# Performance work log

Hardware: AMD Instinct MI355X
Metric: run time of the kernel (lower is better)

Reference implementation:

```python
import jax, jax.numpy as jnp
import numpy as np
import math

L, N, D = 1024, 64, 64
O = 1024

def setup_inputs() -> dict:
    key = jax.random.key(0)
    k1, k2 = jax.random.split(key)
    x = jax.random.normal(k1, (L, N, D), dtype=jnp.float32)
    upfold = jax.random.normal(k2, (O, N, D), dtype=jnp.float32)
    return {"x": x, "upfold": upfold}

def reference(x, upfold):
    # x: [L, N, D], upfold: [O, N, D]
    d = x.shape[-1]
    scale = 1.0 / math.sqrt(d)
    # affinities: [L, O, N]
    affinities = jnp.einsum('lnd,ond->lon', x, upfold) * scale
    # weighted sum with (sigmoid - 0.5) weights: [L, N, D]
    features = jnp.einsum('lon,ond->lnd', jax.nn.sigmoid(affinities) - 0.5, upfold)
    return features
```

## Files before the change

kernel.cpp:

```cpp
#include <hip/hip_runtime.h>
#include <stdint.h>

#define L_DIM 1024
#define N_DIM 64
#define D_DIM 64
#define O_DIM 1024
#define ND    4096
#define NT    8

typedef float    floatx16 __attribute__((ext_vector_type(16)));
typedef _Float16 half8    __attribute__((ext_vector_type(8)));
typedef _Float16 h2       __attribute__((ext_vector_type(2)));
typedef __fp16   fp16x2   __attribute__((ext_vector_type(2)));

#define IMG_TILE 19
#undef IMG_TILE
#define UB_BYTES  9216
#define UTT_BYTES 9728
#define IMG_BYTES (UB_BYTES + UTT_BYTES)
#define WS_NEEDED ((size_t)N_DIM * 16 * IMG_BYTES)

#define BUF_STRIDE_FB 17920

__device__ __forceinline__ uint32_t pkh2(float a, float b) {
    fp16x2 p = __builtin_amdgcn_cvt_pkrtz(a, b);
    return __builtin_bit_cast(uint32_t, p);
}

__device__ __forceinline__ half8 mk_frag(uint32_t a, uint32_t b, uint32_t c, uint32_t d) {
    union { uint32_t u[4]; half8 v; } U;
    U.u[0] = a; U.u[1] = b; U.u[2] = c; U.u[3] = d;
    return U.v;
}

__device__ __forceinline__ uint32_t psig(float s0, float s1) {
    const h2 HI = {(_Float16)41.6f,        (_Float16)41.6f};
    const h2 LO = {(_Float16)-41.6f,       (_Float16)-41.6f};
    const h2 SC = {(_Float16)0.0625f,      (_Float16)0.0625f};
    const h2 C0 = {(_Float16)0.03099238f,  (_Float16)0.03099238f};
    const h2 C1 = {(_Float16)-0.00842090f, (_Float16)-0.00842090f};
    const h2 C2 = {(_Float16)0.00151845f,  (_Float16)0.00151845f};
    const h2 C3 = {(_Float16)-1.02197e-4f, (_Float16)-1.02197e-4f};
    h2 s = __builtin_bit_cast(h2, pkh2(s0, s1));
    s = __builtin_elementwise_min(s, HI);
    s = __builtin_elementwise_max(s, LO);
    h2 ha = s * SC;
    h2 v  = ha * ha;
    h2 w  = C2 + v * C3;
    w     = C1 + v * w;
    w     = C0 + v * w;
    h2 f  = s * w;
    return __builtin_bit_cast(uint32_t, f);
}

__device__ __forceinline__ void load_tile(const float* ubase, int ot,
                                          int r8, int c, float4* va, float4* vb) {
    const float* pr = ubase + (size_t)(ot * 64 + 2 * r8) * ND + 4 * c;
    #pragma unroll
    for (int j = 0; j < 2; ++j) {
        va[j] = *(const float4*)(pr + (size_t)(32 * j) * ND);
        vb[j] = *(const float4*)(pr + (size_t)(32 * j) * ND + ND);
    }
}

__device__ __forceinline__ void gll16(const unsigned char* g, unsigned char* l) {
    __builtin_amdgcn_global_load_lds(
        (const __attribute__((address_space(1))) void*)g,
        (__attribute__((address_space(3))) void*)l, 16, 0, 0);
}

__global__ void __launch_bounds__(256)
conv_kernel(const float* __restrict__ up, unsigned char* __restrict__ img)
{
    const int tid = threadIdx.x;
    const int r8  = tid >> 4;
    const int c   = tid & 15;
    const int n   = blockIdx.x;
    const int ot  = blockIdx.y;

    const float* ubase = up + (size_t)n * D_DIM;
    float4 va[2], vb[2];
    load_tile(ubase, ot, r8, c, va, vb);

    unsigned char* tb = img + (size_t)(n * 16 + ot) * IMG_BYTES;
    uint16_t (*Ub)[72]  = (uint16_t (*)[72])tb;
    uint32_t (*UtT)[38] = (uint32_t (*)[38])(tb + UB_BYTES);

    #pragma unroll
    for (int j = 0; j < 2; ++j) {
        *(uint2*)&Ub[2*r8 + 32*j][4*c] =
            make_uint2(pkh2(va[j].x, va[j].y), pkh2(va[j].z, va[j].w));
        *(uint2*)&Ub[2*r8 + 32*j + 1][4*c] =
            make_uint2(pkh2(vb[j].x, vb[j].y), pkh2(vb[j].z, vb[j].w));
        const int op = r8 + 16*j;
        UtT[4*c + 0][op] = pkh2(va[j].x, vb[j].x);
        UtT[4*c + 1][op] = pkh2(va[j].y, vb[j].y);
        UtT[4*c + 2][op] = pkh2(va[j].z, vb[j].z);
        UtT[4*c + 3][op] = pkh2(va[j].w, vb[j].w);
    }
}

__global__ void __launch_bounds__(512, 4)
corr_kernel_g(const float* __restrict__ x, const unsigned char* __restrict__ img,
              float* __restrict__ out)
{
    __shared__ __align__(16) unsigned char smem[4 * IMG_BYTES];

    const int tid  = threadIdx.x;
    const int lane = tid & 63;
    const int wid  = tid >> 6;
    const int team = wid >> 2;
    const int tw   = wid & 3;
    const int l31  = lane & 31;
    const int h    = lane >> 5;
    const int ttid = tid & 255;
    const int n    = blockIdx.x;
    const int lb   = blockIdx.y;
    const int lw   = lb * 128 + tw * 32 + l31;

    const int ob = team * NT;
    unsigned char* tsmem = smem + team * 2 * IMG_BYTES;
    const unsigned char* gimg = img + (size_t)n * 16 * IMG_BYTES;

    half8 Xf[4];
    {
        float (*Xs)[68] = (float (*)[68])smem;
        const int xr = tid >> 2;
        const int xq = tid & 3;
        const float* xsrc = x + (size_t)(lb * 128 + xr) * ND + n * D_DIM;
        #pragma unroll
        for (int j = 0; j < 4; ++j) {
            const int f4i = xq * 4 + j;
            *(float4*)&Xs[xr][4 * f4i] = *(const float4*)(xsrc + 4 * f4i);
        }
        __syncthreads();
        const int rl = tw * 32 + l31;
        #pragma unroll
        for (int kk = 0; kk < 4; ++kk) {
            float4 f1 = *(const float4*)&Xs[rl][16 * kk + 8 * h];
            float4 f2 = *(const float4*)&Xs[rl][16 * kk + 8 * h + 4];
            Xf[kk] = mk_frag(pkh2(f1.x, f1.y), pkh2(f1.z, f1.w),
                             pkh2(f2.x, f2.y), pkh2(f2.z, f2.w));
        }
        __syncthreads();
    }

    {
        const unsigned char* g0 = gimg + (size_t)ob * IMG_BYTES;
        #pragma unroll
        for (int i = 0; i < 4; ++i)
            gll16(g0 + ttid * 16 + i * 4096, tsmem + tw * 1024 + i * 4096);
        if (ttid < 160)
            gll16(g0 + ttid * 16 + 16384, tsmem + tw * 1024 + 16384);
    }
    __syncthreads();

    floatx16 F0, F1;
    #pragma unroll
    for (int i = 0; i < 16; ++i) { F0[i] = 0.0f; F1[i] = 0.0f; }

    for (int ot = 0; ot < NT; ++ot) {
        const int b = ot & 1;
        const unsigned char* bufc = tsmem + b * IMG_BYTES;
        unsigned char*       bufn = tsmem + (b ^ 1) * IMG_BYTES;
        const uint16_t (*Ub)[72] = (const uint16_t (*)[72])bufc;
        const uint32_t* utT      = (const uint32_t*)(bufc + UB_BYTES);

        if (ot + 1 < NT) {
            const unsigned char* gn = gimg + (size_t)(ob + ot + 1) * IMG_BYTES;
            #pragma unroll
            for (int i = 0; i < 4; ++i)
                gll16(gn + ttid * 16 + i * 4096, bufn + tw * 1024 + i * 4096);
            if (ttid < 160)
                gll16(gn + ttid * 16 + 16384, bufn + tw * 1024 + 16384);
        }

        half8 A0k[4], A1k[4];
        #pragma unroll
        for (int kk = 0; kk < 4; ++kk) {
            A0k[kk] = *(const half8*)&Ub[l31][16 * kk + 8 * h];
            A1k[kk] = *(const half8*)&Ub[32 + l31][16 * kk + 8 * h];
        }

        floatx16 S0, S1;
        #pragma unroll
        for (int i = 0; i < 16; ++i) { S0[i] = 0.0f; S1[i] = 0.0f; }
        #pragma unroll
        for (int kk = 0; kk < 4; ++kk) {
            S0 = __builtin_amdgcn_mfma_f32_32x32x16_f16(A0k[kk], Xf[kk], S0, 0, 0, 0);
            S1 = __builtin_amdgcn_mfma_f32_32x32x16_f16(A1k[kk], Xf[kk], S1, 0, 0, 0);
        }

        uint32_t P[16];
        #pragma unroll
        for (int m = 0; m < 8; ++m) P[m]     = psig(S0[2*m], S0[2*m+1]);
        #pragma unroll
        for (int m = 0; m < 8; ++m) P[8 + m] = psig(S1[2*m], S1[2*m+1]);

        uint32_t R[8];
        #pragma unroll
        for (int c2 = 0; c2 < 4; ++c2) {
            const uint32_t* Q = P + (c2 >> 1) * 8;
            const int t4 = (c2 & 1) * 4;
            R[2*c2]   = __shfl_xor(h ? Q[t4]     : Q[t4 + 2], 32);
            R[2*c2+1] = __shfl_xor(h ? Q[t4 + 1] : Q[t4 + 3], 32);
        }
        #pragma unroll
        for (int c2 = 0; c2 < 4; ++c2) {
            const uint32_t* Q = P + (c2 >> 1) * 8;
            const int t4 = (c2 & 1) * 4;
            half8 B = h ? mk_frag(R[2*c2], R[2*c2+1], Q[t4 + 2], Q[t4 + 3])
                        : mk_frag(Q[t4], Q[t4 + 1], R[2*c2], R[2*c2+1]);
            const int opb = 8 * c2 + 4 * h;
            const uint32_t* r0 = utT + l31 * 38;
            const uint32_t* r1 = utT + (32 + l31) * 38;
            uint2 q0 = *(const uint2*)(r0 + opb);
            uint2 q1 = *(const uint2*)(r0 + opb + 2);
            uint2 q2 = *(const uint2*)(r1 + opb);
            uint2 q3 = *(const uint2*)(r1 + opb + 2);
            half8 A0 = mk_frag(q0.x, q0.y, q1.x, q1.y);
            half8 A1 = mk_frag(q2.x, q2.y, q3.x, q3.y);
            F0 = __builtin_amdgcn_mfma_f32_32x32x16_f16(A0, B, F0, 0, 0, 0);
            F1 = __builtin_amdgcn_mfma_f32_32x32x16_f16(A1, B, F1, 0, 0, 0);
        }
        __syncthreads();
    }

    {
        float (*Fs)[68] = (float (*)[68])smem;
        const int row = tw * 32 + l31;
        if (team == 1) {
            #pragma unroll
            for (int q = 0; q < 4; ++q) {
                float4 a; a.x = F0[4*q]; a.y = F0[4*q+1]; a.z = F0[4*q+2]; a.w = F0[4*q+3];
                *(float4*)&Fs[row][8*q + 4*h] = a;
                float4 bq; bq.x = F1[4*q]; bq.y = F1[4*q+1]; bq.z = F1[4*q+2]; bq.w = F1[4*q+3];
                *(float4*)&Fs[row][32 + 8*q + 4*h] = bq;
            }
        }
        __syncthreads();
        if (team == 0) {
            float* op = out + (size_t)lw * ND + n * D_DIM;
            #pragma unroll
            for (int q = 0; q < 4; ++q) {
                float4 t0 = *(const float4*)&Fs[row][8*q + 4*h];
                float4 a; a.x = F0[4*q]   + t0.x; a.y = F0[4*q+1] + t0.y;
                          a.z = F0[4*q+2] + t0.z; a.w = F0[4*q+3] + t0.w;
                *(float4*)(op + 8*q + 4*h) = a;
                float4 t1 = *(const float4*)&Fs[row][32 + 8*q + 4*h];
                float4 bq; bq.x = F1[4*q]   + t1.x; bq.y = F1[4*q+1] + t1.y;
                           bq.z = F1[4*q+2] + t1.z; bq.w = F1[4*q+3] + t1.w;
                *(float4*)(op + 32 + 8*q + 4*h) = bq;
            }
        }
    }
}

__global__ void __launch_bounds__(512, 4)
corr_kernel_fb(const float* __restrict__ x, const float* __restrict__ up,
               float* __restrict__ out)
{
    __shared__ __align__(16) unsigned char smem[4 * BUF_STRIDE_FB];

    const int tid  = threadIdx.x;
    const int lane = tid & 63;
    const int wid  = tid >> 6;
    const int team = wid >> 2;
    const int tw   = wid & 3;
    const int l31  = lane & 31;
    const int h    = lane >> 5;
    const int ttid = tid & 255;
    const int r8   = ttid >> 4;
    const int c    = ttid & 15;
    const int n    = blockIdx.x;
    const int lb   = blockIdx.y;
    const int lw   = lb * 128 + tw * 32 + l31;

    const float* ubase = up + (size_t)n * D_DIM;
    const int ob = team * NT;
    unsigned char* tsmem = smem + team * 2 * BUF_STRIDE_FB;

    float4 va[2], vb[2];
    load_tile(ubase, ob + 0, r8, c, va, vb);

    half8 Xf[4];
    {
        float (*Xs)[68] = (float (*)[68])smem;
        const int xr = tid >> 2;
        const int xq = tid & 3;
        const float* xsrc = x + (size_t)(lb * 128 + xr) * ND + n * D_DIM;
        #pragma unroll
        for (int j = 0; j < 4; ++j) {
            const int f4i = xq * 4 + j;
            *(float4*)&Xs[xr][4 * f4i] = *(const float4*)(xsrc + 4 * f4i);
        }
        __syncthreads();
        const int rl = tw * 32 + l31;
        #pragma unroll
        for (int kk = 0; kk < 4; ++kk) {
            float4 f1 = *(const float4*)&Xs[rl][16 * kk + 8 * h];
            float4 f2 = *(const float4*)&Xs[rl][16 * kk + 8 * h + 4];
            Xf[kk] = mk_frag(pkh2(f1.x, f1.y), pkh2(f1.z, f1.w),
                             pkh2(f2.x, f2.y), pkh2(f2.z, f2.w));
        }
        __syncthreads();
    }

    #pragma unroll
    for (int j = 0; j < 2; ++j) {
        uint16_t (*Ub)[72]  = (uint16_t (*)[72])(tsmem);
        uint32_t (*Ut2)[68] = (uint32_t (*)[68])(tsmem + 9216);
        *(uint2*)&Ub[2*r8 + 32*j][4*c] =
            make_uint2(pkh2(va[j].x, va[j].y), pkh2(va[j].z, va[j].w));
        *(uint2*)&Ub[2*r8 + 32*j + 1][4*c] =
            make_uint2(pkh2(vb[j].x, vb[j].y), pkh2(vb[j].z, vb[j].w));
        *(uint4*)&Ut2[r8 + 16*j][4*c] =
            make_uint4(pkh2(va[j].x, vb[j].x), pkh2(va[j].y, vb[j].y),
                       pkh2(va[j].z, vb[j].z), pkh2(va[j].w, vb[j].w));
    }
    load_tile(ubase, ob + 1, r8, c, va, vb);
    __syncthreads();

    floatx16 F0, F1;
    #pragma unroll
    for (int i = 0; i < 16; ++i) { F0[i] = 0.0f; F1[i] = 0.0f; }

    for (int ot = 0; ot < NT; ++ot) {
        const int b = ot & 1;
        uint16_t (*Ub)[72]   = (uint16_t (*)[72])(tsmem + b * BUF_STRIDE_FB);
        const uint32_t* utp  = (const uint32_t*)(tsmem + b * BUF_STRIDE_FB + 9216);
        uint16_t (*Ubn)[72]  = (uint16_t (*)[72])(tsmem + (b ^ 1) * BUF_STRIDE_FB);
        uint32_t (*Ut2n)[68] = (uint32_t (*)[68])(tsmem + (b ^ 1) * BUF_STRIDE_FB + 9216);

        half8 A0k[4], A1k[4];
        #pragma unroll
        for (int kk = 0; kk < 4; ++kk) {
            A0k[kk] = *(const half8*)&Ub[l31][16 * kk + 8 * h];
            A1k[kk] = *(const half8*)&Ub[32 + l31][16 * kk + 8 * h];
        }

        if (ot + 1 < NT) {
            #pragma unroll
            for (int j = 0; j < 2; ++j) {
                *(uint2*)&Ubn[2*r8 + 32*j][4*c] =
                    make_uint2(pkh2(va[j].x, va[j].y), pkh2(va[j].z, va[j].w));
                *(uint2*)&Ubn[2*r8 + 32*j + 1][4*c] =
                    make_uint2(pkh2(vb[j].x, vb[j].y), pkh2(vb[j].z, vb[j].w));
                *(uint4*)&Ut2n[r8 + 16*j][4*c] =
                    make_uint4(pkh2(va[j].x, vb[j].x), pkh2(va[j].y, vb[j].y),
                               pkh2(va[j].z, vb[j].z), pkh2(va[j].w, vb[j].w));
            }
        }
        if (ot + 2 < NT)
            load_tile(ubase, ob + ot + 2, r8, c, va, vb);

        floatx16 S0, S1;
        #pragma unroll
        for (int i = 0; i < 16; ++i) { S0[i] = 0.0f; S1[i] = 0.0f; }
        #pragma unroll
        for (int kk = 0; kk < 4; ++kk) {
            S0 = __builtin_amdgcn_mfma_f32_32x32x16_f16(A0k[kk], Xf[kk], S0, 0, 0, 0);
            S1 = __builtin_amdgcn_mfma_f32_32x32x16_f16(A1k[kk], Xf[kk], S1, 0, 0, 0);
        }

        uint32_t P[16];
        #pragma unroll
        for (int m = 0; m < 8; ++m) P[m]     = psig(S0[2*m], S0[2*m+1]);
        #pragma unroll
        for (int m = 0; m < 8; ++m) P[8 + m] = psig(S1[2*m], S1[2*m+1]);

        uint32_t R[8];
        #pragma unroll
        for (int c2 = 0; c2 < 4; ++c2) {
            const uint32_t* Q = P + (c2 >> 1) * 8;
            const int t4 = (c2 & 1) * 4;
            R[2*c2]   = __shfl_xor(h ? Q[t4]     : Q[t4 + 2], 32);
            R[2*c2+1] = __shfl_xor(h ? Q[t4 + 1] : Q[t4 + 3], 32);
        }
        #pragma unroll
        for (int c2 = 0; c2 < 4; ++c2) {
            const uint32_t* Q = P + (c2 >> 1) * 8;
            const int t4 = (c2 & 1) * 4;
            half8 B = h ? mk_frag(R[2*c2], R[2*c2+1], Q[t4 + 2], Q[t4 + 3])
                        : mk_frag(Q[t4], Q[t4 + 1], R[2*c2], R[2*c2+1]);
            const int opb = 8 * c2 + 4 * h;
            uint32_t a0[4], a1[4];
            #pragma unroll
            for (int k = 0; k < 4; ++k) {
                a0[k] = utp[(opb + k) * 68 + l31];
                a1[k] = utp[(opb + k) * 68 + 32 + l31];
            }
            half8 A0 = mk_frag(a0[0], a0[1], a0[2], a0[3]);
            half8 A1 = mk_frag(a1[0], a1[1], a1[2], a1[3]);
            F0 = __builtin_amdgcn_mfma_f32_32x32x16_f16(A0, B, F0, 0, 0, 0);
            F1 = __builtin_amdgcn_mfma_f32_32x32x16_f16(A1, B, F1, 0, 0, 0);
        }
        __syncthreads();
    }

    {
        float (*Fs)[68] = (float (*)[68])smem;
        const int row = tw * 32 + l31;
        if (team == 1) {
            #pragma unroll
            for (int q = 0; q < 4; ++q) {
                float4 a; a.x = F0[4*q]; a.y = F0[4*q+1]; a.z = F0[4*q+2]; a.w = F0[4*q+3];
                *(float4*)&Fs[row][8*q + 4*h] = a;
                float4 bq; bq.x = F1[4*q]; bq.y = F1[4*q+1]; bq.z = F1[4*q+2]; bq.w = F1[4*q+3];
                *(float4*)&Fs[row][32 + 8*q + 4*h] = bq;
            }
        }
        __syncthreads();
        if (team == 0) {
            float* op = out + (size_t)lw * ND + n * D_DIM;
            #pragma unroll
            for (int q = 0; q < 4; ++q) {
                float4 t0 = *(const float4*)&Fs[row][8*q + 4*h];
                float4 a; a.x = F0[4*q]   + t0.x; a.y = F0[4*q+1] + t0.y;
                          a.z = F0[4*q+2] + t0.z; a.w = F0[4*q+3] + t0.w;
                *(float4*)(op + 8*q + 4*h) = a;
                float4 t1 = *(const float4*)&Fs[row][32 + 8*q + 4*h];
                float4 bq; bq.x = F1[4*q]   + t1.x; bq.y = F1[4*q+1] + t1.y;
                           bq.z = F1[4*q+2] + t1.z; bq.w = F1[4*q+3] + t1.w;
                *(float4*)(op + 32 + 8*q + 4*h) = bq;
            }
        }
    }
}

extern "C" void kernel_launch(void* const* d_in, const int* in_sizes, int n_in,
                              void* d_out, int out_size, void* d_ws, size_t ws_size,
                              hipStream_t stream)
{
    const float* x  = (const float*)d_in[0];
    const float* up = (const float*)d_in[1];
    float* out      = (float*)d_out;

    if (d_ws != nullptr && ws_size >= WS_NEEDED) {
        unsigned char* img = (unsigned char*)d_ws;
        conv_kernel<<<dim3(N_DIM, 16), dim3(256), 0, stream>>>(up, img);
        corr_kernel_g<<<dim3(N_DIM, L_DIM / 128), dim3(512), 0, stream>>>(x, img, out);
    } else {
        corr_kernel_fb<<<dim3(N_DIM, L_DIM / 128), dim3(512), 0, stream>>>(x, up, out);
    }
}
```

Before: 109.5 us.

## Restructure corr kernel to load half the upfold images into LDS at once

```diff
diff --git a/kernel.cpp b/kernel.cpp
--- a/kernel.cpp
+++ b/kernel.cpp
@@ -13,11 +13,10 @@
 typedef _Float16 h2       __attribute__((ext_vector_type(2)));
 typedef __fp16   fp16x2   __attribute__((ext_vector_type(2)));
 
-#define IMG_TILE 19
-#undef IMG_TILE
 #define UB_BYTES  9216
 #define UTT_BYTES 9728
 #define IMG_BYTES (UB_BYTES + UTT_BYTES)
+#define HALF_BYTES (8 * IMG_BYTES)
 #define WS_NEEDED ((size_t)N_DIM * 16 * IMG_BYTES)
 
 #define BUF_STRIDE_FB 17920
@@ -69,6 +68,15 @@
         (__attribute__((address_space(3))) void*)l, 16, 0, 0);
 }
 
+__device__ __forceinline__ void dma_half(const unsigned char* gh, unsigned char* lds,
+                                         int wid, int lane) {
+    #pragma unroll
+    for (int k = 0; k < 18; ++k)
+        gll16(gh + wid * 1024 + k * 8192 + lane * 16, lds + wid * 1024 + k * 8192);
+    if (wid < 4)
+        gll16(gh + 147456 + wid * 1024 + lane * 16, lds + 147456 + wid * 1024);
+}
+
 __global__ void __launch_bounds__(256)
 conv_kernel(const float* __restrict__ up, unsigned char* __restrict__ img)
 {
@@ -100,41 +108,36 @@
     }
 }
 
-__global__ void __launch_bounds__(512, 4)
-corr_kernel_g(const float* __restrict__ x, const unsigned char* __restrict__ img,
-              float* __restrict__ out)
+__global__ void __launch_bounds__(512, 2)
+corr_kernel_g2(const float* __restrict__ x, const unsigned char* __restrict__ img,
+               float* __restrict__ out)
 {
-    __shared__ __align__(16) unsigned char smem[4 * IMG_BYTES];
+    __shared__ __align__(16) unsigned char smem[HALF_BYTES];
 
     const int tid  = threadIdx.x;
     const int lane = tid & 63;
     const int wid  = tid >> 6;
-    const int team = wid >> 2;
-    const int tw   = wid & 3;
     const int l31  = lane & 31;
     const int h    = lane >> 5;
-    const int ttid = tid & 255;
     const int n    = blockIdx.x;
     const int lb   = blockIdx.y;
-    const int lw   = lb * 128 + tw * 32 + l31;
-
-    const int ob = team * NT;
-    unsigned char* tsmem = smem + team * 2 * IMG_BYTES;
+    const int lw   = lb * 256 + wid * 32 + l31;
+
     const unsigned char* gimg = img + (size_t)n * 16 * IMG_BYTES;
 
     half8 Xf[4];
     {
         float (*Xs)[68] = (float (*)[68])smem;
-        const int xr = tid >> 2;
-        const int xq = tid & 3;
-        const float* xsrc = x + (size_t)(lb * 128 + xr) * ND + n * D_DIM;
-        #pragma unroll
-        for (int j = 0; j < 4; ++j) {
-            const int f4i = xq * 4 + j;
+        const int xr = tid >> 1;
+        const int xh = tid & 1;
+        const float* xsrc = x + (size_t)(lb * 256 + xr) * ND + n * D_DIM;
+        #pragma unroll
+        for (int j = 0; j < 8; ++j) {
+            const int f4i = xh * 8 + j;
             *(float4*)&Xs[xr][4 * f4i] = *(const float4*)(xsrc + 4 * f4i);
         }
         __syncthreads();
-        const int rl = tw * 32 + l31;
+        const int rl = wid * 32 + l31;
         #pragma unroll
         for (int kk = 0; kk < 4; ++kk) {
             float4 f1 = *(const float4*)&Xs[rl][16 * kk + 8 * h];
@@ -145,114 +148,84 @@
         __syncthreads();
     }
 
-    {
-        const unsigned char* g0 = gimg + (size_t)ob * IMG_BYTES;
-        #pragma unroll
-        for (int i = 0; i < 4; ++i)
-            gll16(g0 + ttid * 16 + i * 4096, tsmem + tw * 1024 + i * 4096);
-        if (ttid < 160)
-            gll16(g0 + ttid * 16 + 16384, tsmem + tw * 1024 + 16384);
-    }
+    dma_half(gimg, smem, wid, lane);
     __syncthreads();
 
     floatx16 F0, F1;
     #pragma unroll
     for (int i = 0; i < 16; ++i) { F0[i] = 0.0f; F1[i] = 0.0f; }
 
-    for (int ot = 0; ot < NT; ++ot) {
-        const int b = ot & 1;
-        const unsigned char* bufc = tsmem + b * IMG_BYTES;
-        unsigned char*       bufn = tsmem + (b ^ 1) * IMG_BYTES;
-        const uint16_t (*Ub)[72] = (const uint16_t (*)[72])bufc;
-        const uint32_t* utT      = (const uint32_t*)(bufc + UB_BYTES);
-
-        if (ot + 1 < NT) {
-            const unsigned char* gn = gimg + (size_t)(ob + ot + 1) * IMG_BYTES;
-            #pragma unroll
-            for (int i = 0; i < 4; ++i)
-                gll16(gn + ttid * 16 + i * 4096, bufn + tw * 1024 + i * 4096);
-            if (ttid < 160)
-                gll16(gn + ttid * 16 + 16384, bufn + tw * 1024 + 16384);
-        }
-
-        half8 A0k[4], A1k[4];
-        #pragma unroll
-        for (int kk = 0; kk < 4; ++kk) {
-            A0k[kk] = *(const half8*)&Ub[l31][16 * kk + 8 * h];
-            A1k[kk] = *(const half8*)&Ub[32 + l31][16 * kk + 8 * h];
-        }
-
-        floatx16 S0, S1;
-        #pragma unroll
-        for (int i = 0; i < 16; ++i) { S0[i] = 0.0f; S1[i] = 0.0f; }
-        #pragma unroll
-        for (int kk = 0; kk < 4; ++kk) {
-            S0 = __builtin_amdgcn_mfma_f32_32x32x16_f16(A0k[kk], Xf[kk], S0, 0, 0, 0);
-            S1 = __builtin_amdgcn_mfma_f32_32x32x16_f16(A1k[kk], Xf[kk], S1, 0, 0, 0);
-        }
-
-        uint32_t P[16];
-        #pragma unroll
-        for (int m = 0; m < 8; ++m) P[m]     = psig(S0[2*m], S0[2*m+1]);
-        #pragma unroll
-        for (int m = 0; m < 8; ++m) P[8 + m] = psig(S1[2*m], S1[2*m+1]);
-
-        uint32_t R[8];
-        #pragma unroll
-        for (int c2 = 0; c2 < 4; ++c2) {
-            const uint32_t* Q = P + (c2 >> 1) * 8;
-            const int t4 = (c2 & 1) * 4;
-            R[2*c2]   = __shfl_xor(h ? Q[t4]     : Q[t4 + 2], 32);
-            R[2*c2+1] = __shfl_xor(h ? Q[t4 + 1] : Q[t4 + 3], 32);
-        }
-        #pragma unroll
-        for (int c2 = 0; c2 < 4; ++c2) {
-            const uint32_t* Q = P + (c2 >> 1) * 8;
-            const int t4 = (c2 & 1) * 4;
-            half8 B = h ? mk_frag(R[2*c2], R[2*c2+1], Q[t4 + 2], Q[t4 + 3])
-                        : mk_frag(Q[t4], Q[t4 + 1], R[2*c2], R[2*c2+1]);
-            const int opb = 8 * c2 + 4 * h;
-            const uint32_t* r0 = utT + l31 * 38;
-            const uint32_t* r1 = utT + (32 + l31) * 38;
-            uint2 q0 = *(const uint2*)(r0 + opb);
-            uint2 q1 = *(const uint2*)(r0 + opb + 2);
-            uint2 q2 = *(const uint2*)(r1 + opb);
-            uint2 q3 = *(const uint2*)(r1 + opb + 2);
-            half8 A0 = mk_frag(q0.x, q0.y, q1.x, q1.y);
-            half8 A1 = mk_frag(q2.x, q2.y, q3.x, q3.y);
-            F0 = __builtin_amdgcn_mfma_f32_32x32x16_f16(A0, B, F0, 0, 0, 0);
-            F1 = __builtin_amdgcn_mfma_f32_32x32x16_f16(A1, B, F1, 0, 0, 0);
-        }
-        __syncthreads();
-    }
-
-    {
-        float (*Fs)[68] = (float (*)[68])smem;
-        const int row = tw * 32 + l31;
-        if (team == 1) {
-            #pragma unroll
-            for (int q = 0; q < 4; ++q) {
-                float4 a; a.x = F0[4*q]; a.y = F0[4*q+1]; a.z = F0[4*q+2]; a.w = F0[4*q+3];
-                *(float4*)&Fs[row][8*q + 4*h] = a;
-                float4 bq; bq.x = F1[4*q]; bq.y = F1[4*q+1]; bq.z = F1[4*q+2]; bq.w = F1[4*q+3];
-                *(float4*)&Fs[row][32 + 8*q + 4*h] = bq;
-            }
-        }
-        __syncthreads();
-        if (team == 0) {
-            float* op = out + (size_t)lw * ND + n * D_DIM;
-            #pragma unroll
-            for (int q = 0; q < 4; ++q) {
-                float4 t0 = *(const float4*)&Fs[row][8*q + 4*h];
-                float4 a; a.x = F0[4*q]   + t0.x; a.y = F0[4*q+1] + t0.y;
-                          a.z = F0[4*q+2] + t0.z; a.w = F0[4*q+3] + t0.w;
-                *(float4*)(op + 8*q + 4*h) = a;
-                float4 t1 = *(const float4*)&Fs[row][32 + 8*q + 4*h];
-                float4 bq; bq.x = F1[4*q]   + t1.x; bq.y = F1[4*q+1] + t1.y;
-                           bq.z = F1[4*q+2] + t1.z; bq.w = F1[4*q+3] + t1.w;
-                *(float4*)(op + 32 + 8*q + 4*h) = bq;
-            }
-        }
+    for (int hb = 0; hb < 2; ++hb) {
+        if (hb == 1) {
+            __syncthreads();
+            dma_half(gimg + HALF_BYTES, smem, wid, lane);
+            __syncthreads();
+        }
+
+        for (int i = 0; i < 8; ++i) {
+            const int ti = (wid + i) & 7;
+            const unsigned char* tb = smem + (size_t)ti * IMG_BYTES;
+            const uint16_t (*Ub)[72] = (const uint16_t (*)[72])tb;
+            const uint32_t* utT      = (const uint32_t*)(tb + UB_BYTES);
+
+            half8 A0k[4], A1k[4];
+            #pragma unroll
+            for (int kk = 0; kk < 4; ++kk) {
+                A0k[kk] = *(const half8*)&Ub[l31][16 * kk + 8 * h];
+                A1k[kk] = *(const half8*)&Ub[32 + l31][16 * kk + 8 * h];
+            }
+
+            floatx16 S0, S1;
+            #pragma unroll
+            for (int i2 = 0; i2 < 16; ++i2) { S0[i2] = 0.0f; S1[i2] = 0.0f; }
+            #pragma unroll
+            for (int kk = 0; kk < 4; ++kk) {
+                S0 = __builtin_amdgcn_mfma_f32_32x32x16_f16(A0k[kk], Xf[kk], S0, 0, 0, 0);
+                S1 = __builtin_amdgcn_mfma_f32_32x32x16_f16(A1k[kk], Xf[kk], S1, 0, 0, 0);
+            }
+
+            uint32_t P[16];
+            #pragma unroll
+            for (int m = 0; m < 8; ++m) P[m]     = psig(S0[2*m], S0[2*m+1]);
+            #pragma unroll
+            for (int m = 0; m < 8; ++m) P[8 + m] = psig(S1[2*m], S1[2*m+1]);
+
+            uint32_t R[8];
+            #pragma unroll
+            for (int c2 = 0; c2 < 4; ++c2) {
+                const uint32_t* Q = P + (c2 >> 1) * 8;
+                const int t4 = (c2 & 1) * 4;
+                R[2*c2]   = __shfl_xor(h ? Q[t4]     : Q[t4 + 2], 32);
+                R[2*c2+1] = __shfl_xor(h ? Q[t4 + 1] : Q[t4 + 3], 32);
+            }
+            #pragma unroll
+            for (int c2 = 0; c2 < 4; ++c2) {
+                const uint32_t* Q = P + (c2 >> 1) * 8;
+                const int t4 = (c2 & 1) * 4;
+                half8 B = h ? mk_frag(R[2*c2], R[2*c2+1], Q[t4 + 2], Q[t4 + 3])
+                            : mk_frag(Q[t4], Q[t4 + 1], R[2*c2], R[2*c2+1]);
+                const int opb = 8 * c2 + 4 * h;
+                const uint32_t* r0 = utT + l31 * 38;
+                const uint32_t* r1 = utT + (32 + l31) * 38;
+                uint2 q0 = *(const uint2*)(r0 + opb);
+                uint2 q1 = *(const uint2*)(r0 + opb + 2);
+                uint2 q2 = *(const uint2*)(r1 + opb);
+                uint2 q3 = *(const uint2*)(r1 + opb + 2);
+                half8 A0 = mk_frag(q0.x, q0.y, q1.x, q1.y);
+                half8 A1 = mk_frag(q2.x, q2.y, q3.x, q3.y);
+                F0 = __builtin_amdgcn_mfma_f32_32x32x16_f16(A0, B, F0, 0, 0, 0);
+                F1 = __builtin_amdgcn_mfma_f32_32x32x16_f16(A1, B, F1, 0, 0, 0);
+            }
+        }
+    }
+
+    float* op = out + (size_t)lw * ND + n * D_DIM;
+    #pragma unroll
+    for (int q = 0; q < 4; ++q) {
+        float4 a; a.x = F0[4*q]; a.y = F0[4*q+1]; a.z = F0[4*q+2]; a.w = F0[4*q+3];
+        *(float4*)(op + 8*q + 4*h) = a;
+        float4 bq; bq.x = F1[4*q]; bq.y = F1[4*q+1]; bq.z = F1[4*q+2]; bq.w = F1[4*q+3];
+        *(float4*)(op + 32 + 8*q + 4*h) = bq;
     }
 }
 
@@ -439,7 +412,7 @@
     if (d_ws != nullptr && ws_size >= WS_NEEDED) {
         unsigned char* img = (unsigned char*)d_ws;
         conv_kernel<<<dim3(N_DIM, 16), dim3(256), 0, stream>>>(up, img);
-        corr_kernel_g<<<dim3(N_DIM, L_DIM / 128), dim3(512), 0, stream>>>(x, img, out);
+        corr_kernel_g2<<<dim3(N_DIM, L_DIM / 256), dim3(512), 0, stream>>>(x, img, out);
     } else {
         corr_kernel_fb<<<dim3(N_DIM, L_DIM / 128), dim3(512), 0, stream>>>(x, up, out);
     }
```

Result: no change. 111.0 us (+1.4%).

## Read upfold fp16 tiles directly from global memory instead of LDS staging

Applied to the files above, without the earlier changes.

```diff
diff --git a/kernel.cpp b/kernel.cpp
--- a/kernel.cpp
+++ b/kernel.cpp
@@ -13,8 +13,6 @@
 typedef _Float16 h2       __attribute__((ext_vector_type(2)));
 typedef __fp16   fp16x2   __attribute__((ext_vector_type(2)));
 
-#define IMG_TILE 19
-#undef IMG_TILE
 #define UB_BYTES  9216
 #define UTT_BYTES 9728
 #define IMG_BYTES (UB_BYTES + UTT_BYTES)
@@ -63,12 +61,6 @@
     }
 }
 
-__device__ __forceinline__ void gll16(const unsigned char* g, unsigned char* l) {
-    __builtin_amdgcn_global_load_lds(
-        (const __attribute__((address_space(1))) void*)g,
-        (__attribute__((address_space(3))) void*)l, 16, 0, 0);
-}
-
 __global__ void __launch_bounds__(256)
 conv_kernel(const float* __restrict__ up, unsigned char* __restrict__ img)
 {
@@ -101,10 +93,10 @@
 }
 
 __global__ void __launch_bounds__(512, 4)
-corr_kernel_g(const float* __restrict__ x, const unsigned char* __restrict__ img,
+corr_kernel_r(const float* __restrict__ x, const unsigned char* __restrict__ img,
               float* __restrict__ out)
 {
-    __shared__ __align__(16) unsigned char smem[4 * IMG_BYTES];
+    __shared__ __align__(16) float Xs[128][68];
 
     const int tid  = threadIdx.x;
     const int lane = tid & 63;
@@ -113,18 +105,14 @@
     const int tw   = wid & 3;
     const int l31  = lane & 31;
     const int h    = lane >> 5;
-    const int ttid = tid & 255;
     const int n    = blockIdx.x;
     const int lb   = blockIdx.y;
     const int lw   = lb * 128 + tw * 32 + l31;
 
-    const int ob = team * NT;
-    unsigned char* tsmem = smem + team * 2 * IMG_BYTES;
     const unsigned char* gimg = img + (size_t)n * 16 * IMG_BYTES;
 
     half8 Xf[4];
     {
-        float (*Xs)[68] = (float (*)[68])smem;
         const int xr = tid >> 2;
         const int xq = tid & 3;
         const float* xsrc = x + (size_t)(lb * 128 + xr) * ND + n * D_DIM;
@@ -145,75 +133,45 @@
         __syncthreads();
     }
 
-    {
-        const unsigned char* g0 = gimg + (size_t)ob * IMG_BYTES;
-        #pragma unroll
-        for (int i = 0; i < 4; ++i)
-            gll16(g0 + ttid * 16 + i * 4096, tsmem + tw * 1024 + i * 4096);
-        if (ttid < 160)
-            gll16(g0 + ttid * 16 + 16384, tsmem + tw * 1024 + 16384);
-    }
-    __syncthreads();
-
     floatx16 F0, F1;
     #pragma unroll
     for (int i = 0; i < 16; ++i) { F0[i] = 0.0f; F1[i] = 0.0f; }
 
-    for (int ot = 0; ot < NT; ++ot) {
-        const int b = ot & 1;
-        const unsigned char* bufc = tsmem + b * IMG_BYTES;
-        unsigned char*       bufn = tsmem + (b ^ 1) * IMG_BYTES;
-        const uint16_t (*Ub)[72] = (const uint16_t (*)[72])bufc;
-        const uint32_t* utT      = (const uint32_t*)(bufc + UB_BYTES);
-
-        if (ot + 1 < NT) {
-            const unsigned char* gn = gimg + (size_t)(ob + ot + 1) * IMG_BYTES;
-            #pragma unroll
-            for (int i = 0; i < 4; ++i)
-                gll16(gn + ttid * 16 + i * 4096, bufn + tw * 1024 + i * 4096);
-            if (ttid < 160)
-                gll16(gn + ttid * 16 + 16384, bufn + tw * 1024 + 16384);
-        }
-
-        half8 A0k[4], A1k[4];
-        #pragma unroll
-        for (int kk = 0; kk < 4; ++kk) {
-            A0k[kk] = *(const half8*)&Ub[l31][16 * kk + 8 * h];
-            A1k[kk] = *(const half8*)&Ub[32 + l31][16 * kk + 8 * h];
-        }
-
-        floatx16 S0, S1;
-        #pragma unroll
-        for (int i = 0; i < 16; ++i) { S0[i] = 0.0f; S1[i] = 0.0f; }
-        #pragma unroll
-        for (int kk = 0; kk < 4; ++kk) {
-            S0 = __builtin_amdgcn_mfma_f32_32x32x16_f16(A0k[kk], Xf[kk], S0, 0, 0, 0);
-            S1 = __builtin_amdgcn_mfma_f32_32x32x16_f16(A1k[kk], Xf[kk], S1, 0, 0, 0);
-        }
-
-        uint32_t P[16];
-        #pragma unroll
-        for (int m = 0; m < 8; ++m) P[m]     = psig(S0[2*m], S0[2*m+1]);
-        #pragma unroll
-        for (int m = 0; m < 8; ++m) P[8 + m] = psig(S1[2*m], S1[2*m+1]);
-
-        uint32_t R[8];
-        #pragma unroll
-        for (int c2 = 0; c2 < 4; ++c2) {
-            const uint32_t* Q = P + (c2 >> 1) * 8;
-            const int t4 = (c2 & 1) * 4;
-            R[2*c2]   = __shfl_xor(h ? Q[t4]     : Q[t4 + 2], 32);
-            R[2*c2+1] = __shfl_xor(h ? Q[t4 + 1] : Q[t4 + 3], 32);
-        }
-        #pragma unroll
-        for (int c2 = 0; c2 < 4; ++c2) {
-            const uint32_t* Q = P + (c2 >> 1) * 8;
-            const int t4 = (c2 & 1) * 4;
-            half8 B = h ? mk_frag(R[2*c2], R[2*c2+1], Q[t4 + 2], Q[t4 + 3])
-                        : mk_frag(Q[t4], Q[t4 + 1], R[2*c2], R[2*c2+1]);
-            const int opb = 8 * c2 + 4 * h;
-            const uint32_t* r0 = utT + l31 * 38;
-            const uint32_t* r1 = utT + (32 + l31) * 38;
+    for (int ot = 0; ot < 16; ++ot) {
+        const unsigned char* tb = gimg + (size_t)ot * IMG_BYTES;
+
+        const unsigned char* ubp = tb + (size_t)(team * 32 + l31) * 144 + h * 16;
+        half8 Ak[4];
+        #pragma unroll
+        for (int kk = 0; kk < 4; ++kk)
+            Ak[kk] = *(const half8*)(ubp + kk * 32);
+
+        floatx16 S;
+        #pragma unroll
+        for (int i2 = 0; i2 < 16; ++i2) S[i2] = 0.0f;
+        #pragma unroll
+        for (int kk = 0; kk < 4; ++kk)
+            S = __builtin_amdgcn_mfma_f32_32x32x16_f16(Ak[kk], Xf[kk], S, 0, 0, 0);
+
+        uint32_t P[8];
+        #pragma unroll
+        for (int m = 0; m < 8; ++m) P[m] = psig(S[2*m], S[2*m+1]);
+
+        uint32_t R[4];
+        #pragma unroll
+        for (int c2 = 0; c2 < 2; ++c2) {
+            const int t4 = c2 * 4;
+            R[2*c2]   = __shfl_xor(h ? P[t4]     : P[t4 + 2], 32);
+            R[2*c2+1] = __shfl_xor(h ? P[t4 + 1] : P[t4 + 3], 32);
+        }
+        const uint32_t* r0 = (const uint32_t*)(tb + UB_BYTES) + l31 * 38;
+        const uint32_t* r1 = r0 + 32 * 38;
+        #pragma unroll
+        for (int c2 = 0; c2 < 2; ++c2) {
+            const int t4 = c2 * 4;
+            half8 B = h ? mk_frag(R[2*c2], R[2*c2+1], P[t4 + 2], P[t4 + 3])
+                        : mk_frag(P[t4], P[t4 + 1], R[2*c2], R[2*c2+1]);
+            const int opb = team * 16 + 8 * c2 + 4 * h;
             uint2 q0 = *(const uint2*)(r0 + opb);
             uint2 q1 = *(const uint2*)(r0 + opb + 2);
             uint2 q2 = *(const uint2*)(r1 + opb);
@@ -223,19 +181,17 @@
             F0 = __builtin_amdgcn_mfma_f32_32x32x16_f16(A0, B, F0, 0, 0, 0);
             F1 = __builtin_amdgcn_mfma_f32_32x32x16_f16(A1, B, F1, 0, 0, 0);
         }
-        __syncthreads();
     }
 
     {
-        float (*Fs)[68] = (float (*)[68])smem;
         const int row = tw * 32 + l31;
         if (team == 1) {
             #pragma unroll
             for (int q = 0; q < 4; ++q) {
                 float4 a; a.x = F0[4*q]; a.y = F0[4*q+1]; a.z = F0[4*q+2]; a.w = F0[4*q+3];
-                *(float4*)&Fs[row][8*q + 4*h] = a;
+                *(float4*)&Xs[row][8*q + 4*h] = a;
                 float4 bq; bq.x = F1[4*q]; bq.y = F1[4*q+1]; bq.z = F1[4*q+2]; bq.w = F1[4*q+3];
-                *(float4*)&Fs[row][32 + 8*q + 4*h] = bq;
+                *(float4*)&Xs[row][32 + 8*q + 4*h] = bq;
             }
         }
         __syncthreads();
@@ -243,11 +199,11 @@
             float* op = out + (size_t)lw * ND + n * D_DIM;
             #pragma unroll
             for (int q = 0; q < 4; ++q) {
-                float4 t0 = *(const float4*)&Fs[row][8*q + 4*h];
+                float4 t0 = *(const float4*)&Xs[row][8*q + 4*h];
                 float4 a; a.x = F0[4*q]   + t0.x; a.y = F0[4*q+1] + t0.y;
                           a.z = F0[4*q+2] + t0.z; a.w = F0[4*q+3] + t0.w;
                 *(float4*)(op + 8*q + 4*h) = a;
-                float4 t1 = *(const float4*)&Fs[row][32 + 8*q + 4*h];
+                float4 t1 = *(const float4*)&Xs[row][32 + 8*q + 4*h];
                 float4 bq; bq.x = F1[4*q]   + t1.x; bq.y = F1[4*q+1] + t1.y;
                            bq.z = F1[4*q+2] + t1.z; bq.w = F1[4*q+3] + t1.w;
                 *(float4*)(op + 32 + 8*q + 4*h) = bq;
@@ -439,7 +395,7 @@
     if (d_ws != nullptr && ws_size >= WS_NEEDED) {
         unsigned char* img = (unsigned char*)d_ws;
         conv_kernel<<<dim3(N_DIM, 16), dim3(256), 0, stream>>>(up, img);
-        corr_kernel_g<<<dim3(N_DIM, L_DIM / 128), dim3(512), 0, stream>>>(x, img, out);
+        corr_kernel_r<<<dim3(N_DIM, L_DIM / 128), dim3(512), 0, stream>>>(x, img, out);
     } else {
         corr_kernel_fb<<<dim3(N_DIM, L_DIM / 128), dim3(512), 0, stream>>>(x, up, out);
     }
```

New measurement: 122.9 us. +12.3%, slower.
